# Optimization experiments

Hardware: AMD Instinct MI355X
Metric: run time of the kernel (lower is better)

The kernel has to match this reference:

```python
import jax, jax.numpy as jnp
import numpy as np

B, H, W = 16, 16, 16
DIM = 768
NH = 8
HD = DIM // NH
NEXP = 8
TOPK = 2
DSTATE = 1
DTRANK = 4
KDIR = 4


def setup_inputs() -> dict:
    key = jax.random.key(0)
    ks = jax.random.split(key, 16)
    s = 1.0 / float(np.sqrt(DIM))
    inp = {
        'x': jax.random.normal(ks[0], (B, H, W, DIM)),
        'sa_in_w': jax.random.normal(ks[1], (3 * DIM, DIM)) * s,
        'sa_in_b': jnp.zeros((3 * DIM,)),
        'sa_out_w': jax.random.normal(ks[2], (DIM, DIM)) * s,
        'sa_out_b': jnp.zeros((DIM,)),
        'ca_in_w': jax.random.normal(ks[3], (2 * DIM, DIM)) * s,
        'ca_in_b': jnp.zeros((2 * DIM,)),
        'expert_queries': jax.random.normal(ks[4], (NEXP, DIM)) * s,
        'e_in_w': jax.random.normal(ks[5], (NEXP, 2 * DIM, DIM)) * s,
        'e_in_b': jnp.zeros((NEXP, 2 * DIM)),
        'e_conv_w': jax.random.normal(ks[6], (NEXP, DIM, 1, 3, 3)) / 3.0,
        'e_conv_b': jnp.zeros((NEXP, DIM)),
        'e_xproj_w': jax.random.normal(ks[7], (NEXP, KDIR, DTRANK + 2 * DSTATE, DIM)) * s,
        'e_dtproj_w': jax.random.normal(ks[8], (NEXP, KDIR, DIM, DTRANK)) * 0.1,
        'e_dtproj_b': jax.random.uniform(ks[9], (NEXP, KDIR, DIM), minval=-4.0, maxval=-2.0),
        'e_Alog': jax.random.uniform(ks[10], (NEXP, KDIR, DIM, DSTATE), minval=0.0, maxval=1.0),
        'e_D': jnp.ones((NEXP, KDIR, DIM)),
        'e_ln_scale': jnp.ones((NEXP, DIM)),
        'e_ln_bias': jnp.zeros((NEXP, DIM)),
    }
    return {k: v.astype(jnp.float32) for k, v in inp.items()}


def _selective_scan(xs, Wx, Wdt, bdt, Alog, D):
    # xs: [B, L, d]; Wx: [R+2N, d]; Wdt: [d, R]; Alog: [d, N]; D: [d]
    dbl = jnp.einsum('bld,ed->ble', xs, Wx)
    dt = jax.nn.softplus(jnp.einsum('blr,dr->bld', dbl[..., :DTRANK], Wdt) + bdt)
    Bm = dbl[..., DTRANK:DTRANK + DSTATE]
    Cm = dbl[..., DTRANK + DSTATE:]
    A = -jnp.exp(Alog)  # [d, N]

    def step(h, t):
        dt_t, B_t, C_t, x_t = t  # [b,d],[b,N],[b,N],[b,d]
        h = jnp.exp(dt_t[:, :, None] * A) * h + (dt_t * x_t)[:, :, None] * B_t[:, None, :]
        return h, jnp.einsum('bdn,bn->bd', h, C_t)

    b, L, d = xs.shape
    h0 = jnp.zeros((b, d, DSTATE), xs.dtype)
    tm = lambda a: jnp.moveaxis(a, 1, 0)
    _, ys = jax.lax.scan(step, h0, (tm(dt), tm(Bm), tm(Cm), tm(xs)))
    return jnp.moveaxis(ys, 0, 1) + D * xs


def _expert(in_w, in_b, conv_w, conv_b, xproj_w, dtp_w, dtp_b, Alog, D, ln_s, ln_b, x):
    b = x.shape[0]
    xz = jnp.einsum('bhwc,oc->bhwo', x, in_w) + in_b
    xc, z = jnp.split(xz, 2, axis=-1)
    xn = jax.lax.conv_general_dilated(jnp.transpose(xc, (0, 3, 1, 2)), conv_w,
                                      (1, 1), ((1, 1), (1, 1)), feature_group_count=DIM)
    xc = jax.nn.silu(jnp.transpose(xn + conv_b[None, :, None, None], (0, 2, 3, 1)))
    L = H * W
    xh = xc.reshape(b, L, DIM)                              # row-major 'h'
    xv = jnp.transpose(xc, (0, 2, 1, 3)).reshape(b, L, DIM)  # col-major 'v'
    seqs = jnp.stack([xh, xh[:, ::-1], xv, xv[:, ::-1]])     # [4, b, L, d]
    ys = jax.vmap(_selective_scan)(seqs, xproj_w, dtp_w, dtp_b, Alog, D)
    yv = ys[2] + ys[3][:, ::-1]
    yv = jnp.transpose(yv.reshape(b, W, H, DIM), (0, 2, 1, 3)).reshape(b, L, DIM)
    y = (ys[0] + ys[1][:, ::-1] + yv).reshape(b, H, W, DIM)
    mu = y.mean(-1, keepdims=True)
    var = ((y - mu) ** 2).mean(-1, keepdims=True)
    y = (y - mu) * jax.lax.rsqrt(var + 1e-5) * ln_s + ln_b   # out_norm (LayerNorm)
    y = y * jax.nn.silu(z)
    return y.mean((1, 2))  # AdaptiveAvgPool2d((1,1)) -> [b, DIM]


def _forward(x, sa_in_w, sa_in_b, sa_out_w, sa_out_b, ca_in_w, ca_in_b, expert_queries,
             e_in_w, e_in_b, e_conv_w, e_conv_b, e_xproj_w, e_dtproj_w, e_dtproj_b,
             e_Alog, e_D, e_ln_scale, e_ln_bias):
    b = x.shape[0]
    L = H * W
    scale = 1.0 / float(np.sqrt(HD))
    xs = x.reshape(b, L, DIM)
    # spatial self-attention (eval mode: dropout off)
    qkv = xs @ sa_in_w.T + sa_in_b
    q, k, v = [a.reshape(b, L, NH, HD) for a in jnp.split(qkv, 3, -1)]
    att = jax.nn.softmax(jnp.einsum('bqhd,bkhd->bhqk', q, k) * scale, -1)
    ctx = jnp.einsum('bhqk,bkhd->bqhd', att, v).reshape(b, L, DIM) @ sa_out_w.T + sa_out_b
    # expert cross-attention: only head-averaged attention weights are used
    q2 = (ctx @ ca_in_w[:DIM].T + ca_in_b[:DIM]).reshape(b, L, NH, HD)
    k2 = (expert_queries @ ca_in_w[DIM:].T + ca_in_b[DIM:]).reshape(NEXP, NH, HD)
    aw = jax.nn.softmax(jnp.einsum('blhd,ehd->bhle', q2, k2) * scale, -1).mean(1)  # [b,L,E]
    gate = jax.nn.softmax(aw.mean(1), -1)  # [b, E]
    tk_scores, tk_idx = jax.lax.top_k(gate, TOPK)
    wgt = jax.nn.softmax(tk_scores, -1)
    # dense expert compute (all experts on all samples), then gather top-k
    all_out = jax.vmap(_expert, in_axes=(0,) * 11 + (None,))(
        e_in_w, e_in_b, e_conv_w, e_conv_b, e_xproj_w, e_dtproj_w, e_dtproj_b,
        e_Alog, e_D, e_ln_scale, e_ln_bias, x)  # [E, b, DIM]
    per_b = jnp.transpose(all_out, (1, 0, 2))  # [b, E, DIM]
    sel = jnp.take_along_axis(per_b, tk_idx[:, :, None], axis=1)  # [b, K, DIM]
    return jnp.sum(wgt[:, :, None] * sel, axis=1)  # [b, DIM]


def reference(x, sa_in_w, sa_in_b, sa_out_w, sa_out_b, ca_in_w, ca_in_b, expert_queries,
              e_in_w, e_in_b, e_conv_w, e_conv_b, e_xproj_w, e_dtproj_w, e_dtproj_b,
              e_Alog, e_D, e_ln_scale, e_ln_bias):
    return _forward(x, sa_in_w, sa_in_b, sa_out_w, sa_out_b, ca_in_w, ca_in_b, expert_queries,
                    e_in_w, e_in_b, e_conv_w, e_conv_b, e_xproj_w, e_dtproj_w, e_dtproj_b,
                    e_Alog, e_D, e_ln_scale, e_ln_bias)
```

## Files before the change

### kernel.cpp

```cpp
#include <hip/hip_runtime.h>
#include <hip/hip_bf16.h>


#define LTOK 256
#define DIMC 768

typedef unsigned short ushortt;
typedef __attribute__((ext_vector_type(8))) short bf16x8;
typedef __attribute__((ext_vector_type(4))) float f32x4;

#define LOG2E 1.44269504f
#define LN2   0.69314718f

__device__ __forceinline__ void gld16(const ushortt* gp, ushortt* lp) {
  __builtin_amdgcn_global_load_lds(
      (const __attribute__((address_space(1))) void*)gp,
      (__attribute__((address_space(3))) void*)lp, 16, 0, 0);
}

__device__ __forceinline__ float fexp2(float x) { return __builtin_amdgcn_exp2f(x); }
__device__ __forceinline__ float flog2(float x) { return __builtin_amdgcn_logf(x); }

__device__ __forceinline__ ushortt f2b(float f) {
  union { float f; unsigned u; } c; c.f = f;
  unsigned r = (c.u + 0x7FFFu + ((c.u >> 16) & 1u)) >> 16;
  return (ushortt)r;
}

__global__ __launch_bounds__(256) void mk_mcast4(
    const float* __restrict__ s0, ushortt* __restrict__ d0,
    const float* __restrict__ s1, ushortt* __restrict__ d1,
    const float* __restrict__ s2, ushortt* __restrict__ d2,
    const float* __restrict__ s3, ushortt* __restrict__ d3)
{
  long g = (long)blockIdx.x * 256 + threadIdx.x;
  const float* s; ushortt* dst; long o;
  if (g < 786432)       { s = s0; dst = d0; o = g; }
  else if (g < 1228800) { s = s1; dst = d1; o = g - 786432; }
  else if (g < 1376256) { s = s2; dst = d2; o = g - 1228800; }
  else                  { s = s3; dst = d3; o = g - 1376256; }
  o <<= 2;
  float4 v = *(const float4*)(s + o);
  ushort4 w;
  w.x = f2b(v.x); w.y = f2b(v.y); w.z = f2b(v.z); w.w = f2b(v.w);
  *(ushort4*)(dst + o) = w;
}

__global__ __launch_bounds__(256) void mk_cast(const float* __restrict__ in,
                                               ushortt* __restrict__ outp, long n)
{
  long i = ((long)blockIdx.x * 256 + threadIdx.x) * 4;
  if (i + 3 < n) {
    float4 v = *(const float4*)(in + i);
    ushort4 o;
    o.x = f2b(v.x); o.y = f2b(v.y); o.z = f2b(v.z); o.w = f2b(v.w);
    *(ushort4*)(outp + i) = o;
  }
}

__global__ __launch_bounds__(256) void mk_mfma(
    const ushortt* __restrict__ A, const ushortt* __restrict__ B,
    const float* __restrict__ bias, void* __restrict__ C,
    int K, int lda, int ldb, int ldc,
    int zdiv, long sA1, long sA2, long sB1, long sB2, long sC1, long sC2,
    long sBias,
    const int* __restrict__ pairExp, int tilesN,
    int outBf, int splitN, void* __restrict__ C2, int ldc2, int outBf2, int c2vt)
{
  int z = blockIdx.y;
  long aoff, boff, coff, biasoff = 0;
  if (pairExp) {
    int e = pairExp[z];
    aoff = (long)(z >> 1) * sA1; boff = (long)e * sB1;
    coff = (long)z * sC1; biasoff = (long)e * sBias;
  } else {
    int z1 = z / zdiv, z2 = z - z1 * zdiv;
    aoff = (long)z1 * sA1 + (long)z2 * sA2;
    boff = (long)z1 * sB1 + (long)z2 * sB2;
    coff = (long)z1 * sC1 + (long)z2 * sC2;
  }
  int tile = blockIdx.x;
  int tm = tile / tilesN, tn = tile - tm * tilesN;
  long m0 = (long)tm << 7, n0 = (long)tn << 7;

  __shared__ ushortt As[128 * 32];
  __shared__ ushortt Bs[128 * 32];

  int tid = threadIdx.x;
  int lane = tid & 63, wvi = tid >> 6;
  int wr = wvi >> 1, wc = wvi & 1;
  int lm = lane & 15, lg = lane >> 4;

  f32x4 zero4 = {0.f, 0.f, 0.f, 0.f};
  f32x4 acc[4][4];
#pragma unroll
  for (int i = 0; i < 4; i++)
#pragma unroll
    for (int j = 0; j < 4; j++) acc[i][j] = zero4;

  const ushortt* Ab = A + aoff;
  const ushortt* Bb = B + boff;

  int srow = (wvi << 5) + (lane >> 2);
  int sglog = ((lane & 3) ^ ((lane >> 3) & 3)) << 3;
  const ushortt* agp = Ab + (m0 + srow) * lda + sglog;
  const ushortt* bgp = Bb + (n0 + srow) * ldb + sglog;
  ushortt* al0 = &As[(wvi << 5) << 5];
  ushortt* al1 = &As[((wvi << 5) + 16) << 5];
  ushortt* bl0 = &Bs[(wvi << 5) << 5];
  ushortt* bl1 = &Bs[((wvi << 5) + 16) << 5];

  int pswz = (lg ^ ((lm >> 1) & 3)) << 3;
  const ushortt* afp[4];
  const ushortt* bfp[4];
#pragma unroll
  for (int i = 0; i < 4; i++) {
    afp[i] = &As[((wr * 64 + i * 16 + lm) << 5) + pswz];
    bfp[i] = &Bs[((wc * 64 + i * 16 + lm) << 5) + pswz];
  }

  for (int k0 = 0; k0 < K; k0 += 32) {
    gld16(agp, al0);
    gld16(agp + 16 * lda, al1);
    gld16(bgp, bl0);
    gld16(bgp + 16 * ldb, bl1);
    agp += 32; bgp += 32;
    __syncthreads();
    bf16x8 af[4], bfr[4];
#pragma unroll
    for (int i = 0; i < 4; i++) {
      af[i] = *(const bf16x8*)afp[i];
      bfr[i] = *(const bf16x8*)bfp[i];
    }
#pragma unroll
    for (int i = 0; i < 4; i++)
#pragma unroll
      for (int j = 0; j < 4; j++)
        acc[i][j] = __builtin_amdgcn_mfma_f32_16x16x32_bf16(af[i], bfr[j], acc[i][j], 0, 0, 0);
    __syncthreads();
  }

#pragma unroll
  for (int mt = 0; mt < 4; mt++) {
#pragma unroll
    for (int nt = 0; nt < 4; nt++) {
      long grow = m0 + wr * 64 + mt * 16 + lg * 4;
      long gcol = n0 + wc * 64 + nt * 16 + lm;
      float bv = bias ? bias[biasoff + gcol] : 0.f;
      if ((int)gcol < splitN) {
#pragma unroll
        for (int r = 0; r < 4; r++) {
          float v = acc[mt][nt][r] + bv;
          long idx = coff + (grow + r) * ldc + gcol;
          if (outBf) ((ushortt*)C)[idx] = f2b(v);
          else ((float*)C)[idx] = v;
        }
      } else if (c2vt) {
        int cc = (int)gcol - splitN;
        int hh = cc / 96, jj = cc - hh * 96;
#pragma unroll
        for (int r = 0; r < 4; r++) {
          float v = acc[mt][nt][r] + bv;
          long gr = grow + r;
          long b = gr >> 8, t = gr & 255;
          long idx = (((b * 8 + hh) * 128 + jj) << 8) + t;
          ((ushortt*)C2)[idx] = f2b(v);
        }
      } else {
        long col = gcol - splitN;
#pragma unroll
        for (int r = 0; r < 4; r++) {
          float v = acc[mt][nt][r] + bv;
          long idx = coff + (grow + r) * ldc2 + col;
          if (outBf2) ((ushortt*)C2)[idx] = f2b(v);
          else ((float*)C2)[idx] = v;
        }
      }
    }
  }
}

__global__ __launch_bounds__(256) void mk_gemm(
    const float* __restrict__ A, const float* __restrict__ B,
    const float* __restrict__ bias, float* __restrict__ C,
    int M, int N, int K, int lda, int ldb, int ldc, int tilesN)
{
  int tile = blockIdx.x;
  int tm = tile / tilesN, tn = tile - tm * tilesN;
  int m0 = tm << 6, n0 = tn << 6;

  __shared__ float As[16][68];
  __shared__ float Bs[16][68];

  int tid = threadIdx.x;
  int tx = tid & 15, ty = tid >> 4;
  int lrow = tid >> 2;
  int lk = (tid & 3) << 2;

  float acc[4][4];
#pragma unroll
  for (int i = 0; i < 4; i++)
#pragma unroll
    for (int j = 0; j < 4; j++) acc[i][j] = 0.f;

  for (int k0 = 0; k0 < K; k0 += 16) {
    {
      int gm = m0 + lrow;
      float4 v = {0.f, 0.f, 0.f, 0.f};
      if (gm < M) v = *(const float4*)(A + (long)gm * lda + (k0 + lk));
      As[lk + 0][lrow] = v.x; As[lk + 1][lrow] = v.y;
      As[lk + 2][lrow] = v.z; As[lk + 3][lrow] = v.w;
    }
    {
      int gn = n0 + lrow;
      float4 v = {0.f, 0.f, 0.f, 0.f};
      if (gn < N) v = *(const float4*)(B + (long)gn * ldb + (k0 + lk));
      Bs[lk + 0][lrow] = v.x; Bs[lk + 1][lrow] = v.y;
      Bs[lk + 2][lrow] = v.z; Bs[lk + 3][lrow] = v.w;
    }
    __syncthreads();
#pragma unroll
    for (int kk = 0; kk < 16; kk++) {
      float4 a = *(const float4*)&As[kk][ty << 2];
      float4 b = *(const float4*)&Bs[kk][tx << 2];
      acc[0][0] += a.x * b.x; acc[0][1] += a.x * b.y; acc[0][2] += a.x * b.z; acc[0][3] += a.x * b.w;
      acc[1][0] += a.y * b.x; acc[1][1] += a.y * b.y; acc[1][2] += a.y * b.z; acc[1][3] += a.y * b.w;
      acc[2][0] += a.z * b.x; acc[2][1] += a.z * b.y; acc[2][2] += a.z * b.z; acc[2][3] += a.z * b.w;
      acc[3][0] += a.w * b.x; acc[3][1] += a.w * b.y; acc[3][2] += a.w * b.z; acc[3][3] += a.w * b.w;
    }
    __syncthreads();
  }

#pragma unroll
  for (int i = 0; i < 4; i++) {
    int gm = m0 + (ty << 2) + i;
    if (gm >= M) continue;
#pragma unroll
    for (int j = 0; j < 4; j++) {
      int gn = n0 + (tx << 2) + j;
      if (gn >= N) continue;
      float v = acc[i][j];
      if (bias) v += bias[gn];
      C[(long)gm * ldc + gn] = v;
    }
  }
}

__global__ __launch_bounds__(256) void mk_softmax(const float* __restrict__ scores,
                                                  ushortt* __restrict__ att, float scale)
{
  int row = (blockIdx.x << 2) + (threadIdx.x >> 6);
  int lane = threadIdx.x & 63;
  const float* p = scores + (long)row * 256 + (lane << 2);
  float4 v = *(const float4*)p;
  float m = fmaxf(fmaxf(v.x, v.y), fmaxf(v.z, v.w));
#pragma unroll
  for (int o = 32; o; o >>= 1) m = fmaxf(m, __shfl_xor(m, o, 64));
  float sl = scale * LOG2E;
  v.x = fexp2(sl * (v.x - m));
  v.y = fexp2(sl * (v.y - m));
  v.z = fexp2(sl * (v.z - m));
  v.w = fexp2(sl * (v.w - m));
  float s = v.x + v.y + v.z + v.w;
#pragma unroll
  for (int o = 32; o; o >>= 1) s += __shfl_xor(s, o, 64);
  float r = 1.f / s;
  ushort4 o4;
  o4.x = f2b(v.x * r); o4.y = f2b(v.y * r); o4.z = f2b(v.z * r); o4.w = f2b(v.w * r);
  *(ushort4*)(att + (long)row * 256 + (lane << 2)) = o4;
}

__global__ __launch_bounds__(256) void mk_gates(const float* __restrict__ q2,
                                                const float* __restrict__ k2,
                                                float* __restrict__ gacc)
{
  __shared__ float k2p[8 * 808];
  int b = blockIdx.x >> 4, q = blockIdx.x & 15;
  for (int i = threadIdx.x; i < 6144; i += 256) {
    int e = i / 768, rem = i - e * 768;
    int h = rem / 96, j = rem - h * 96;
    k2p[e * 808 + h * 100 + j] = k2[i];
  }
  __syncthreads();
  const float scale = 0.10206207261596577f;
  int wid = threadIdx.x >> 6, lane = threadIdx.x & 63;
  int h = lane >> 3, e = lane & 7;
  const float* kp = &k2p[e * 808 + h * 100];
  float accL = 0.f;
#pragma unroll
  for (int ti = 0; ti < 4; ti++) {
    int l = q * 16 + wid * 4 + ti;
    const float* qh = q2 + ((long)b * LTOK + l) * DIMC + h * 96;
    float sum = 0.f;
#pragma unroll
    for (int j = 0; j < 96; j += 4) {
      float4 qv = *(const float4*)(qh + j);
      float4 kv = *(const float4*)(kp + j);
      sum += qv.x * kv.x + qv.y * kv.y + qv.z * kv.z + qv.w * kv.w;
    }
    float s = sum * scale;
    float mx = s;
#pragma unroll
    for (int o = 1; o <= 4; o <<= 1) mx = fmaxf(mx, __shfl_xor(mx, o, 64));
    float ex = fexp2((s - mx) * LOG2E);
    float se = ex;
#pragma unroll
    for (int o = 1; o <= 4; o <<= 1) se += __shfl_xor(se, o, 64);
    accL += ex / se;
  }
#pragma unroll
  for (int o = 8; o <= 32; o <<= 1) accL += __shfl_xor(accL, o, 64);
  __shared__ float red[4][8];
  if (lane < 8) red[wid][lane] = accL;
  __syncthreads();
  if (threadIdx.x < 8) {
    float v = red[0][threadIdx.x] + red[1][threadIdx.x] +
              red[2][threadIdx.x] + red[3][threadIdx.x];
    atomicAdd(&gacc[b * 8 + threadIdx.x], v);
  }
}

__global__ __launch_bounds__(64) void mk_gatetop(const float* __restrict__ gacc,
                                                 int* __restrict__ pe,
                                                 float* __restrict__ pw)
{
  int b = threadIdx.x;
  if (b >= 16) return;
  float g[8];
  for (int e = 0; e < 8; e++) g[e] = gacc[b * 8 + e] * (1.f / (8.f * 256.f));
  float mx = g[0];
  for (int e = 1; e < 8; e++) mx = fmaxf(mx, g[e]);
  float se = 0.f;
  for (int e = 0; e < 8; e++) { g[e] = expf(g[e] - mx); se += g[e]; }
  for (int e = 0; e < 8; e++) g[e] /= se;
  int i0 = 0;
  for (int e = 1; e < 8; e++) if (g[e] > g[i0]) i0 = e;
  int i1 = (i0 == 0) ? 1 : 0;
  for (int e = 0; e < 8; e++) if (e != i0 && g[e] > g[i1]) i1 = e;
  float w0 = 1.f / (1.f + expf(g[i1] - g[i0]));
  pe[2 * b] = i0; pe[2 * b + 1] = i1;
  pw[2 * b] = w0; pw[2 * b + 1] = 1.f - w0;
}

__global__ __launch_bounds__(768) void mk_conv(const float* __restrict__ xzx,
                                               const float* __restrict__ cw,
                                               const float* __restrict__ cb,
                                               const int* __restrict__ pe,
                                               float* __restrict__ xc)
{
  int blk = blockIdx.x;
  int p = blk >> 8, t = blk & 255;
  int e = pe[p];
  int h = t >> 4, w = t & 15;
  int c = threadIdx.x;
  const float* wp = cw + ((long)e * DIMC + c) * 9;
  float acc = cb[e * DIMC + c];
#pragma unroll
  for (int dh = 0; dh < 3; dh++) {
    int hh = h + dh - 1;
    if (hh < 0 || hh > 15) continue;
#pragma unroll
    for (int dw = 0; dw < 3; dw++) {
      int ww = w + dw - 1;
      if (ww < 0 || ww > 15) continue;
      acc += xzx[((long)p * LTOK + hh * 16 + ww) * DIMC + c] * wp[dh * 3 + dw];
    }
  }
  xc[((long)p * LTOK + t) * DIMC + c] = acc / (1.f + fexp2(-acc * LOG2E));
}

__device__ __forceinline__ int tmap(int dir, int s) {
  if (dir == 0) return s;
  if (dir == 1) return 255 - s;
  if (dir == 2) return ((s & 15) << 4) | (s >> 4);
  int u = 255 - s;
  return ((u & 15) << 4) | (u >> 4);
}

__global__ __launch_bounds__(256) void mk_dbl(const float* __restrict__ xc,
                                              const float* __restrict__ xproj,
                                              const int* __restrict__ pe,
                                              float* __restrict__ dblm)
{
  int p = blockIdx.x >> 6;
  int tq = blockIdx.x & 63;
  int wid = threadIdx.x >> 6, lane = threadIdx.x & 63;
  int m = tq * 4 + wid;
  int e = pe[p];
  const float* xr = xc + ((long)p * LTOK + m) * DIMC;
  const float* wb = xproj + (long)e * 24 * DIMC;
  float4 xv[3];
#pragma unroll
  for (int j = 0; j < 3; j++) xv[j] = *(const float4*)(xr + j * 256 + lane * 4);
  float acc[24];
#pragma unroll
  for (int r = 0; r < 24; r++) {
    const float* wr = wb + r * DIMC;
    float s = 0.f;
#pragma unroll
    for (int j = 0; j < 3; j++) {
      float4 wv = *(const float4*)(wr + j * 256 + lane * 4);
      s += xv[j].x * wv.x + xv[j].y * wv.y + xv[j].z * wv.z + xv[j].w * wv.w;
    }
    acc[r] = s;
  }
#pragma unroll
  for (int r = 0; r < 24; r++)
#pragma unroll
    for (int o = 32; o; o >>= 1) acc[r] += __shfl_xor(acc[r], o, 64);
  if (lane == 0) {
    float* o = dblm + (long)p * 6144;
#pragma unroll
    for (int dd = 0; dd < 4; dd++) {
      int s = tmap(dd, m);
      int ss = ((s & 31) << 3) | (s >> 5);
      float* oa = o + dd * 1024 + ss * 4;
      oa[0] = acc[dd * 6 + 0]; oa[1] = acc[dd * 6 + 1];
      oa[2] = acc[dd * 6 + 2]; oa[3] = acc[dd * 6 + 3];
      float* ob = o + 4096 + dd * 512 + ss * 2;
      ob[0] = acc[dd * 6 + 4]; ob[1] = acc[dd * 6 + 5];
    }
  }
}

__global__ __launch_bounds__(512, 6) void mk_scan(const float* __restrict__ xc,
                                               const float* __restrict__ dblm,
                                               const float* __restrict__ dtw,
                                               const float* __restrict__ dtb,
                                               const float* __restrict__ Alog,
                                               const float* __restrict__ Dp,
                                               const int* __restrict__ pe,
                                               float* __restrict__ yac)
{
  __shared__ __attribute__((aligned(16))) float dtS[4096];
  __shared__ __attribute__((aligned(16))) float bcS[2048];
  __shared__ float yS[256 * 18];
  __shared__ float ahS[32][16][2];
  __shared__ float dsum[16];
  int blk = blockIdx.x;
  int p = blk / 48, cg = blk - p * 48;
  int c0 = cg << 4;
  int e = pe[p];
  int tid = threadIdx.x;
  {
    const float4* src = (const float4*)(dblm + (long)p * 6144);
    float4* dA = (float4*)dtS;
    for (int i = tid; i < 1024; i += 512) dA[i] = src[i];
    if (tid < 512) ((float4*)bcS)[tid] = src[1024 + tid];
  }
  for (int i = tid; i < 256 * 18; i += 512) yS[i] = 0.f;
  if (tid < 16) {
    float s = 0.f;
#pragma unroll
    for (int dd = 0; dd < 4; dd++) s += Dp[(long)(e * 4 + dd) * DIMC + c0 + tid];
    dsum[tid] = s;
  }
  __syncthreads();

  int c = tid & 15;
  int rr = tid >> 4;
  int seg = rr & 7;
  int dir = rr >> 3;
  int d = c0 + c;
  const float* xcp = xc + (long)p * LTOK * DIMC + d;
  long pb = (long)(e * 4 + dir) * DIMC + d;
  float4 wv = *(const float4*)(dtw + pb * 4);
  wv.x *= LOG2E; wv.y *= LOG2E; wv.z *= LOG2E; wv.w *= LOG2E;
  float bdt = dtb[pb] * LOG2E;
  float Ad = -fexp2(Alog[pb] * LOG2E);
  int t0 = seg << 5;
  const float* dtP = &dtS[(dir << 10) + (seg << 2)];
  const float* bcP = &bcS[(dir << 9) + (seg << 1)];

  float h = 0.f, ap = 1.f;
#pragma unroll 1
  for (int tb = 0; tb < 32; tb += 4) {
#pragma unroll
    for (int u = 0; u < 4; u++) {
      int i = tb + u;
      float4 dv = *(const float4*)(dtP + i * 32);
      float2 bc = *(const float2*)(bcP + i * 16);
      int mm = tmap(dir, t0 + i);
      float xv = xcp[(long)mm * DIMC];
      float xl = wv.x * dv.x + wv.y * dv.y + wv.z * dv.z + wv.w * dv.w + bdt;
      float te = fexp2(xl);
      float g = flog2(1.f + te);
      g = (xl > 86.f) ? xl : g;
      float de = fexp2(g * Ad);
      h = de * h + (g * LN2 * bc.x) * xv;
      ap *= de;
    }
    __builtin_amdgcn_sched_barrier(0);
  }
  ahS[rr][c][0] = ap;
  ahS[rr][c][1] = h;
  __syncthreads();

  float hh = 0.f;
  {
    int base = dir << 3;
    float av[8], hv[8];
#pragma unroll
    for (int j = 0; j < 8; j++) {
      av[j] = ahS[base + j][c][0];
      hv[j] = ahS[base + j][c][1];
    }
#pragma unroll
    for (int j = 0; j < 7; j++)
      if (j < seg) hh = av[j] * hh + hv[j];
  }

#pragma unroll 1
  for (int tb = 0; tb < 32; tb += 4) {
#pragma unroll
    for (int u = 0; u < 4; u++) {
      int i = tb + u;
      float4 dv = *(const float4*)(dtP + i * 32);
      float2 bc = *(const float2*)(bcP + i * 16);
      int mm = tmap(dir, t0 + i);
      float xv = xcp[(long)mm * DIMC];
      float xl = wv.x * dv.x + wv.y * dv.y + wv.z * dv.z + wv.w * dv.w + bdt;
      float te = fexp2(xl);
      float g = flog2(1.f + te);
      g = (xl > 86.f) ? xl : g;
      float de = fexp2(g * Ad);
      hh = de * hh + (g * LN2 * bc.x) * xv;
      atomicAdd(&yS[mm * 18 + c + (((mm >> 5) & 1) << 1)], hh * bc.y);
    }
    __builtin_amdgcn_sched_barrier(0);
  }
  __syncthreads();

  const float* xcb = xc + (long)p * LTOK * DIMC + c0;
  float* yp = yac + (long)p * LTOK * DIMC + c0;
  for (int i = tid; i < 4096; i += 512) {
    int t = i >> 4, cz = i & 15;
    yp[(long)t * DIMC + cz] = yS[t * 18 + cz + (((t >> 5) & 1) << 1)] +
        xcb[(long)t * DIMC + cz] * dsum[cz];
  }
}

__global__ __launch_bounds__(256) void mk_lnfin(const float* __restrict__ yac,
                                                const float* __restrict__ xzz,
                                                const float* __restrict__ lns,
                                                const float* __restrict__ lnb,
                                                const int* __restrict__ pe,
                                                float* __restrict__ eo)
{
  int blk = blockIdx.x;
  int p = blk >> 4, ts = blk & 15;
  int e = pe[p];
  int tid = threadIdx.x;
  int wid = tid >> 6, lane = tid & 63;
  float ls[12], lb[12], acc[12];
#pragma unroll
  for (int i = 0; i < 12; i++) {
    int d = i * 64 + lane;
    ls[i] = lns[e * DIMC + d];
    lb[i] = lnb[e * DIMC + d];
    acc[i] = 0.f;
  }
#pragma unroll
  for (int tt = 0; tt < 4; tt++) {
    int t = ts * 16 + wid * 4 + tt;
    const float* yr = yac + ((long)p * LTOK + t) * DIMC;
    const float* zr = xzz + ((long)p * LTOK + t) * DIMC;
    float v[12];
    float s = 0.f;
#pragma unroll
    for (int i = 0; i < 12; i++) { v[i] = yr[i * 64 + lane]; s += v[i]; }
#pragma unroll
    for (int o = 32; o; o >>= 1) s += __shfl_xor(s, o, 64);
    float mu = s * (1.f / 768.f);
    float sq = 0.f;
#pragma unroll
    for (int i = 0; i < 12; i++) { float dlt = v[i] - mu; sq += dlt * dlt; }
#pragma unroll
    for (int o = 32; o; o >>= 1) sq += __shfl_xor(sq, o, 64);
    float rs = rsqrtf(sq * (1.f / 768.f) + 1e-5f);
#pragma unroll
    for (int i = 0; i < 12; i++) {
      float y = (v[i] - mu) * rs * ls[i] + lb[i];
      float z = zr[i * 64 + lane];
      y *= z / (1.f + fexp2(-z * LOG2E));
      acc[i] += y;
    }
  }
  __shared__ float sacc[768];
  for (int j = tid; j < 768; j += 256) sacc[j] = 0.f;
  __syncthreads();
#pragma unroll
  for (int i = 0; i < 12; i++) atomicAdd(&sacc[i * 64 + lane], acc[i]);
  __syncthreads();
  for (int j = tid; j < 768; j += 256) atomicAdd(&eo[(long)p * DIMC + j], sacc[j]);
}

__global__ __launch_bounds__(768) void mk_out(const float* __restrict__ eo,
                                              const float* __restrict__ pw,
                                              float* __restrict__ out)
{
  int b = blockIdx.x, d = threadIdx.x;
  float v = pw[2 * b] * eo[(long)(2 * b) * DIMC + d] +
            pw[2 * b + 1] * eo[(long)(2 * b + 1) * DIMC + d];
  out[b * DIMC + d] = v * (1.f / 256.f);
}

extern "C" void kernel_launch(void* const* d_in, const int* in_sizes, int n_in,
                              void* d_out, int out_size, void* d_ws, size_t ws_size,
                              hipStream_t stream)
{
  const float* x        = (const float*)d_in[0];
  const float* sa_in_w  = (const float*)d_in[1];
  const float* sa_in_b  = (const float*)d_in[2];
  const float* sa_out_w = (const float*)d_in[3];
  const float* sa_out_b = (const float*)d_in[4];
  const float* ca_in_w  = (const float*)d_in[5];
  const float* ca_in_b  = (const float*)d_in[6];
  const float* eq       = (const float*)d_in[7];
  const float* e_in_w   = (const float*)d_in[8];
  const float* e_in_b   = (const float*)d_in[9];
  const float* e_conv_w = (const float*)d_in[10];
  const float* e_conv_b = (const float*)d_in[11];
  const float* e_xproj  = (const float*)d_in[12];
  const float* e_dtw    = (const float*)d_in[13];
  const float* e_dtb    = (const float*)d_in[14];
  const float* e_Alog   = (const float*)d_in[15];
  const float* e_D      = (const float*)d_in[16];
  const float* e_lns    = (const float*)d_in[17];
  const float* e_lnb    = (const float*)d_in[18];
  float* out = (float*)d_out;

  float* ws = (float*)d_ws;
  ushortt* qk_b   = (ushortt*)(ws + 0);
  float*   scores = ws + 6291456;
  ushortt* dump_b = (ushortt*)(ws + 6291456);
  ushortt* ctxa_b = (ushortt*)(ws + 7864320);
  ushortt* att_b  = (ushortt*)(ws + 14680064);
  ushortt* vt_b   = (ushortt*)(ws + 18874368);
  ushortt* xb     = (ushortt*)(ws + 20971520);
  ushortt* wqkv_b = (ushortt*)(ws + 22544384);
  ushortt* saow_b = (ushortt*)(ws + 23429120);
  ushortt* caw_b  = (ushortt*)(ws + 23724032);
  ushortt* ctx_b  = (ushortt*)(ws + 0);
  float*   q2     = ws + 1572864;
  float*   k2     = ws + 25165824;
  int*     pe     = (int*)(ws + 25171968);
  float*   pw     = ws + 25172000;
  float*   eo     = ws + 25172032;
  float*   gacc   = ws + 25393216;
  float*   xz_x   = ws + 0;
  float*   xz_z   = ws + 6291456;
  ushortt* ew_b   = (ushortt*)(ws + 12582912);
  float*   xc     = ws + 12582912;
  float*   yac    = ws + 18874368;
  float*   dblm   = ws + 0;

  const float scale = 0.10206207261596577f;

  mk_mcast4<<<5952, 256, 0, stream>>>(x, xb, sa_in_w, wqkv_b, sa_out_w, saow_b,
                                      ca_in_w, caw_b);
  mk_mfma<<<dim3(576, 1), 256, 0, stream>>>(xb, wqkv_b, sa_in_b, qk_b,
      768, 768, 768, 1536, 1, 0, 0, 0, 0, 0, 0, 0, nullptr, 18,
      1, 1536, vt_b, 0, 1, 1);
  mk_mfma<<<dim3(4, 128), 256, 0, stream>>>(qk_b, qk_b + 768, nullptr, scores,
      96, 1536, 1536, 256, 8, 393216, 96, 393216, 96, 524288, 65536, 0, nullptr, 2,
      0, 1 << 30, nullptr, 0, 0, 0);
  mk_softmax<<<8192, 256, 0, stream>>>(scores, att_b, scale);
  mk_mfma<<<dim3(2, 128), 256, 0, stream>>>(att_b, vt_b, nullptr, ctxa_b,
      256, 256, 256, 768, 8, 524288, 65536, 262144, 32768, 196608, 96, 0, nullptr, 1,
      1, 96, dump_b, 32, 1, 0);
  mk_cast<<<9216, 256, 0, stream>>>(e_in_w, ew_b, 9437184);
  mk_mfma<<<dim3(192, 1), 256, 0, stream>>>(ctxa_b, saow_b, sa_out_b, ctx_b,
      768, 768, 768, 768, 1, 0, 0, 0, 0, 0, 0, 0, nullptr, 6,
      1, 1 << 30, nullptr, 0, 0, 0);
  mk_mfma<<<dim3(192, 1), 256, 0, stream>>>(ctx_b, caw_b, ca_in_b, q2,
      768, 768, 768, 768, 1, 0, 0, 0, 0, 0, 0, 0, nullptr, 6,
      0, 1 << 30, nullptr, 0, 0, 0);
  mk_gemm<<<dim3(12, 1), 256, 0, stream>>>(eq, ca_in_w + 589824, ca_in_b + 768, k2,
      8, 768, 768, 768, 768, 768, 12);
  (void)hipMemsetAsync(gacc, 0, 128 * sizeof(float), stream);
  (void)hipMemsetAsync(eo, 0, 24576 * sizeof(float), stream);
  mk_gates<<<256, 256, 0, stream>>>(q2, k2, gacc);
  mk_gatetop<<<1, 64, 0, stream>>>(gacc, pe, pw);
  mk_mfma<<<dim3(24, 32), 256, 0, stream>>>(xb, ew_b, e_in_b, xz_x,
      768, 768, 768, 768, 1, 196608, 0, 1179648, 0, 196608, 0, 1536, pe, 12,
      0, 768, xz_z, 768, 0, 0);
  mk_conv<<<32 * 256, 768, 0, stream>>>(xz_x, e_conv_w, e_conv_b, pe, xc);
  mk_dbl<<<2048, 256, 0, stream>>>(xc, e_xproj, pe, dblm);
  mk_scan<<<1536, 512, 0, stream>>>(xc, dblm, e_dtw, e_dtb, e_Alog, e_D, pe, yac);
  mk_lnfin<<<512, 256, 0, stream>>>(yac, xz_z, e_lns, e_lnb, pe, eo);
  mk_out<<<16, 768, 0, stream>>>(eo, pw, out);

  (void)in_sizes; (void)n_in; (void)out_size; (void)ws_size;
}
```

Before: 622.4 us.

## Fuse softmax into attention-V kernel, fold memsets, batch conv tokens per block

Replaces the separate softmax plus bf16 attention-matrix GEMM with one kernel. It computes row max and sum from the fp32 scores, normalizes them on the fly into bf16 in shared memory, and multiplies against V held in LDS using MFMA. The two memsets move into existing kernels (the cast kernel and mk_dbl), which removes API launches. The depthwise conv now processes 8 tokens per block with the weights held in registers. Together these cut launches and the att_b round trip, but the scores are read three times per row and the fused kernel is a single-stage, non-pipelined GEMM.

```diff
diff --git a/kernel.cpp b/kernel.cpp
--- a/kernel.cpp
+++ b/kernel.cpp
@@ -31,8 +31,10 @@
     const float* __restrict__ s0, ushortt* __restrict__ d0,
     const float* __restrict__ s1, ushortt* __restrict__ d1,
     const float* __restrict__ s2, ushortt* __restrict__ d2,
-    const float* __restrict__ s3, ushortt* __restrict__ d3)
-{
+    const float* __restrict__ s3, ushortt* __restrict__ d3,
+    float* __restrict__ gacc)
+{
+  if (blockIdx.x == 0 && threadIdx.x < 128) gacc[threadIdx.x] = 0.f;
   long g = (long)blockIdx.x * 256 + threadIdx.x;
   const float* s; ushortt* dst; long o;
   if (g < 786432)       { s = s0; dst = d0; o = g; }
@@ -180,6 +182,108 @@
   }
 }
 
+__global__ __launch_bounds__(256) void mk_attv(const float* __restrict__ scores,
+                                               const ushortt* __restrict__ vt,
+                                               ushortt* __restrict__ ctxa)
+{
+  __shared__ ushortt Vs[96 * 264];
+  __shared__ __attribute__((aligned(16))) ushortt As[128 * 40];
+  int z = blockIdx.y, half = blockIdx.x;
+  int t = threadIdx.x;
+  const float* srow = scores + (long)z * 65536 + (long)half * 128 * 256;
+  const ushortt* vb = vt + (long)z * 32768;
+
+  for (int it = 0; it < 12; it++) {
+    int cch = it * 256 + t;
+    int j = cch >> 5, q = cch & 31;
+    *(uint4*)&Vs[j * 264 + q * 8] = *(const uint4*)(vb + j * 256 + q * 8);
+  }
+
+  int r = t >> 1, hf = t & 1;
+  const float* sp = srow + (long)r * 256 + hf * 128;
+  const float sl = 0.10206207261596577f * LOG2E;
+  float m = -3.4e38f;
+  for (int j = 0; j < 128; j += 4) {
+    float4 v = *(const float4*)(sp + j);
+    m = fmaxf(m, fmaxf(fmaxf(v.x, v.y), fmaxf(v.z, v.w)));
+  }
+  m = fmaxf(m, __shfl_xor(m, 1, 64));
+  float s = 0.f;
+  for (int j = 0; j < 128; j += 4) {
+    float4 v = *(const float4*)(sp + j);
+    s += fexp2(sl * (v.x - m)) + fexp2(sl * (v.y - m)) +
+         fexp2(sl * (v.z - m)) + fexp2(sl * (v.w - m));
+  }
+  s += __shfl_xor(s, 1, 64);
+  float rinv = 1.f / s;
+
+  int lane = t & 63, w = t >> 6;
+  int lm = lane & 15, lg = lane >> 4;
+  f32x4 zero4 = {0.f, 0.f, 0.f, 0.f};
+  f32x4 acc[2][6];
+#pragma unroll
+  for (int i = 0; i < 2; i++)
+#pragma unroll
+    for (int j = 0; j < 6; j++) acc[i][j] = zero4;
+
+  const float* stp = srow + (long)(t >> 1) * 256 + (t & 1) * 16;
+  ushortt* adst = &As[(t >> 1) * 40 + (t & 1) * 16];
+
+  for (int k0 = 0; k0 < 256; k0 += 32) {
+    float4 a0 = *(const float4*)(stp + k0);
+    float4 a1 = *(const float4*)(stp + k0 + 4);
+    float4 a2 = *(const float4*)(stp + k0 + 8);
+    float4 a3 = *(const float4*)(stp + k0 + 12);
+    ushortt pk[16];
+    pk[0]  = f2b(fexp2(sl * (a0.x - m)) * rinv);
+    pk[1]  = f2b(fexp2(sl * (a0.y - m)) * rinv);
+    pk[2]  = f2b(fexp2(sl * (a0.z - m)) * rinv);
+    pk[3]  = f2b(fexp2(sl * (a0.w - m)) * rinv);
+    pk[4]  = f2b(fexp2(sl * (a1.x - m)) * rinv);
+    pk[5]  = f2b(fexp2(sl * (a1.y - m)) * rinv);
+    pk[6]  = f2b(fexp2(sl * (a1.z - m)) * rinv);
+    pk[7]  = f2b(fexp2(sl * (a1.w - m)) * rinv);
+    pk[8]  = f2b(fexp2(sl * (a2.x - m)) * rinv);
+    pk[9]  = f2b(fexp2(sl * (a2.y - m)) * rinv);
+    pk[10] = f2b(fexp2(sl * (a2.z - m)) * rinv);
+    pk[11] = f2b(fexp2(sl * (a2.w - m)) * rinv);
+    pk[12] = f2b(fexp2(sl * (a3.x - m)) * rinv);
+    pk[13] = f2b(fexp2(sl * (a3.y - m)) * rinv);
+    pk[14] = f2b(fexp2(sl * (a3.z - m)) * rinv);
+    pk[15] = f2b(fexp2(sl * (a3.w - m)) * rinv);
+    *(uint4*)adst = *(uint4*)&pk[0];
+    *(uint4*)(adst + 8) = *(uint4*)&pk[8];
+    __syncthreads();
+    bf16x8 af[2], bfr[6];
+#pragma unroll
+    for (int i = 0; i < 2; i++)
+      af[i] = *(const bf16x8*)&As[(w * 32 + i * 16 + lm) * 40 + lg * 8];
+#pragma unroll
+    for (int j = 0; j < 6; j++)
+      bfr[j] = *(const bf16x8*)&Vs[(j * 16 + lm) * 264 + k0 + lg * 8];
+#pragma unroll
+    for (int i = 0; i < 2; i++)
+#pragma unroll
+      for (int j = 0; j < 6; j++)
+        acc[i][j] = __builtin_amdgcn_mfma_f32_16x16x32_bf16(af[i], bfr[j], acc[i][j], 0, 0, 0);
+    __syncthreads();
+  }
+
+  int b = z >> 3, h = z & 7;
+#pragma unroll
+  for (int i = 0; i < 2; i++) {
+#pragma unroll
+    for (int j = 0; j < 6; j++) {
+      int tok = half * 128 + w * 32 + i * 16 + lg * 4;
+      int col = j * 16 + lm;
+#pragma unroll
+      for (int rr2 = 0; rr2 < 4; rr2++) {
+        ctxa[((long)(b * 256 + tok + rr2)) * 768 + h * 96 + col] = f2b(acc[i][j][rr2]);
+      }
+    }
+  }
+}
+
 __global__ __launch_bounds__(256) void mk_gemm(
     const float* __restrict__ A, const float* __restrict__ B,
     const float* __restrict__ bias, float* __restrict__ C,
@@ -244,30 +348,6 @@
       C[(long)gm * ldc + gn] = v;
     }
   }
-}
-
-__global__ __launch_bounds__(256) void mk_softmax(const float* __restrict__ scores,
-                                                  ushortt* __restrict__ att, float scale)
-{
-  int row = (blockIdx.x << 2) + (threadIdx.x >> 6);
-  int lane = threadIdx.x & 63;
-  const float* p = scores + (long)row * 256 + (lane << 2);
-  float4 v = *(const float4*)p;
-  float m = fmaxf(fmaxf(v.x, v.y), fmaxf(v.z, v.w));
-#pragma unroll
-  for (int o = 32; o; o >>= 1) m = fmaxf(m, __shfl_xor(m, o, 64));
-  float sl = scale * LOG2E;
-  v.x = fexp2(sl * (v.x - m));
-  v.y = fexp2(sl * (v.y - m));
-  v.z = fexp2(sl * (v.z - m));
-  v.w = fexp2(sl * (v.w - m));
-  float s = v.x + v.y + v.z + v.w;
-#pragma unroll
-  for (int o = 32; o; o >>= 1) s += __shfl_xor(s, o, 64);
-  float r = 1.f / s;
-  ushort4 o4;
-  o4.x = f2b(v.x * r); o4.y = f2b(v.y * r); o4.z = f2b(v.z * r); o4.w = f2b(v.w * r);
-  *(ushort4*)(att + (long)row * 256 + (lane << 2)) = o4;
 }
 
 __global__ __launch_bounds__(256) void mk_gates(const float* __restrict__ q2,
@@ -349,24 +429,33 @@
                                                float* __restrict__ xc)
 {
   int blk = blockIdx.x;
-  int p = blk >> 8, t = blk & 255;
+  int p = blk >> 5, tg = blk & 31;
   int e = pe[p];
-  int h = t >> 4, w = t & 15;
   int c = threadIdx.x;
   const float* wp = cw + ((long)e * DIMC + c) * 9;
-  float acc = cb[e * DIMC + c];
-#pragma unroll
-  for (int dh = 0; dh < 3; dh++) {
-    int hh = h + dh - 1;
-    if (hh < 0 || hh > 15) continue;
-#pragma unroll
-    for (int dw = 0; dw < 3; dw++) {
-      int ww = w + dw - 1;
-      if (ww < 0 || ww > 15) continue;
-      acc += xzx[((long)p * LTOK + hh * 16 + ww) * DIMC + c] * wp[dh * 3 + dw];
-    }
-  }
-  xc[((long)p * LTOK + t) * DIMC + c] = acc / (1.f + fexp2(-acc * LOG2E));
+  float w9[9];
+#pragma unroll
+  for (int i = 0; i < 9; i++) w9[i] = wp[i];
+  float bias = cb[e * DIMC + c];
+  const float* xb = xzx + (long)p * LTOK * DIMC + c;
+#pragma unroll
+  for (int i = 0; i < 8; i++) {
+    int t = tg * 8 + i;
+    int h = t >> 4, w = t & 15;
+    float acc = bias;
+#pragma unroll
+    for (int dh = 0; dh < 3; dh++) {
+      int hh = h + dh - 1;
+      if (hh < 0 || hh > 15) continue;
+#pragma unroll
+      for (int dw = 0; dw < 3; dw++) {
+        int ww = w + dw - 1;
+        if (ww < 0 || ww > 15) continue;
+        acc += xb[(long)(hh * 16 + ww) * DIMC] * w9[dh * 3 + dw];
+      }
+    }
+    xc[((long)p * LTOK + t) * DIMC + c] = acc / (1.f + fexp2(-acc * LOG2E));
+  }
 }
 
 __device__ __forceinline__ int tmap(int dir, int s) {
@@ -380,8 +469,10 @@
 __global__ __launch_bounds__(256) void mk_dbl(const float* __restrict__ xc,
                                               const float* __restrict__ xproj,
                                               const int* __restrict__ pe,
-                                              float* __restrict__ dblm)
-{
+                                              float* __restrict__ dblm,
+                                              float* __restrict__ eo)
+{
+  if (blockIdx.x < 96) eo[blockIdx.x * 256 + threadIdx.x] = 0.f;
   int p = blockIdx.x >> 6;
   int tq = blockIdx.x & 63;
   int wid = threadIdx.x >> 6, lane = threadIdx.x & 63;
@@ -633,9 +724,7 @@
   float* ws = (float*)d_ws;
   ushortt* qk_b   = (ushortt*)(ws + 0);
   float*   scores = ws + 6291456;
-  ushortt* dump_b = (ushortt*)(ws + 6291456);
-  ushortt* ctxa_b = (ushortt*)(ws + 7864320);
-  ushortt* att_b  = (ushortt*)(ws + 14680064);
+  ushortt* ctxa_b = (ushortt*)(ws + 14680064);
   ushortt* vt_b   = (ushortt*)(ws + 18874368);
   ushortt* xb     = (ushortt*)(ws + 20971520);
   ushortt* wqkv_b = (ushortt*)(ws + 22544384);
@@ -655,38 +744,31 @@
   float*   yac    = ws + 18874368;
   float*   dblm   = ws + 0;
 
-  const float scale = 0.10206207261596577f;
-
   mk_mcast4<<<5952, 256, 0, stream>>>(x, xb, sa_in_w, wqkv_b, sa_out_w, saow_b,
-                                      ca_in_w, caw_b);
+                                      ca_in_w, caw_b, gacc);
   mk_mfma<<<dim3(576, 1), 256, 0, stream>>>(xb, wqkv_b, sa_in_b, qk_b,
       768, 768, 768, 1536, 1, 0, 0, 0, 0, 0, 0, 0, nullptr, 18,
       1, 1536, vt_b, 0, 1, 1);
   mk_mfma<<<dim3(4, 128), 256, 0, stream>>>(qk_b, qk_b + 768, nullptr, scores,
       96, 1536, 1536, 256, 8, 393216, 96, 393216, 96, 524288, 65536, 0, nullptr, 2,
       0, 1 << 30, nullptr, 0, 0, 0);
-  mk_softmax<<<8192, 256, 0, stream>>>(scores, att_b, scale);
-  mk_mfma<<<dim3(2, 128), 256, 0, stream>>>(att_b, vt_b, nullptr, ctxa_b,
-      256, 256, 256, 768, 8, 524288, 65536, 262144, 32768, 196608, 96, 0, nullptr, 1,
-      1, 96, dump_b, 32, 1, 0);
-  mk_cast<<<9216, 256, 0, stream>>>(e_in_w, ew_b, 9437184);
+  mk_attv<<<dim3(2, 128), 256, 0, stream>>>(scores, vt_b, ctxa_b);
   mk_mfma<<<dim3(192, 1), 256, 0, stream>>>(ctxa_b, saow_b, sa_out_b, ctx_b,
       768, 768, 768, 768, 1, 0, 0, 0, 0, 0, 0, 0, nullptr, 6,
       1, 1 << 30, nullptr, 0, 0, 0);
+  mk_cast<<<9216, 256, 0, stream>>>(e_in_w, ew_b, 9437184);
   mk_mfma<<<dim3(192, 1), 256, 0, stream>>>(ctx_b, caw_b, ca_in_b, q2,
       768, 768, 768, 768, 1, 0, 0, 0, 0, 0, 0, 0, nullptr, 6,
       0, 1 << 30, nullptr, 0, 0, 0);
   mk_gemm<<<dim3(12, 1), 256, 0, stream>>>(eq, ca_in_w + 589824, ca_in_b + 768, k2,
       8, 768, 768, 768, 768, 768, 12);
-  (void)hipMemsetAsync(gacc, 0, 128 * sizeof(float), stream);
-  (void)hipMemsetAsync(eo, 0, 24576 * sizeof(float), stream);
   mk_gates<<<256, 256, 0, stream>>>(q2, k2, gacc);
   mk_gatetop<<<1, 64, 0, stream>>>(gacc, pe, pw);
   mk_mfma<<<dim3(24, 32), 256, 0, stream>>>(xb, ew_b, e_in_b, xz_x,
       768, 768, 768, 768, 1, 196608, 0, 1179648, 0, 196608, 0, 1536, pe, 12,
       0, 768, xz_z, 768, 0, 0);
-  mk_conv<<<32 * 256, 768, 0, stream>>>(xz_x, e_conv_w, e_conv_b, pe, xc);
-  mk_dbl<<<2048, 256, 0, stream>>>(xc, e_xproj, pe, dblm);
+  mk_conv<<<1024, 768, 0, stream>>>(xz_x, e_conv_w, e_conv_b, pe, xc);
+  mk_dbl<<<2048, 256, 0, stream>>>(xc, e_xproj, pe, dblm, eo);
   mk_scan<<<1536, 512, 0, stream>>>(xc, dblm, e_dtw, e_dtb, e_Alog, e_D, pe, yac);
   mk_lnfin<<<512, 256, 0, stream>>>(yac, xz_z, e_lns, e_lnb, pe, eo);
   mk_out<<<16, 768, 0, stream>>>(eo, pw, out);
```

Result: faster. 580.1 us (-6.8%).
